# Kernel tuning notes

Measured on AMD Instinct MI355X. Metric: run time of the kernel, lower is better.

Reference implementation:

```python
import jax, jax.numpy as jnp
import numpy as np

N_LAYERS = 2
N_HIGHWAY = 2
WIDTH = 4
D = 256
B, S = 32, 1024


def setup_inputs() -> dict:
    key = jax.random.key(0)
    ks = jax.random.split(key, 10)
    inputs = jax.random.normal(ks[0], (B, S, D), dtype=jnp.float32)
    fwd_pad = jax.random.normal(ks[1], (N_LAYERS, WIDTH, D), dtype=jnp.float32) / np.sqrt(D)
    bwd_pad = jax.random.normal(ks[2], (N_LAYERS, WIDTH, D), dtype=jnp.float32) / np.sqrt(D)
    fwd_w = jax.random.normal(ks[3], (N_LAYERS, WIDTH + 1), dtype=jnp.float32)
    bwd_w = jax.random.normal(ks[4], (N_LAYERS, WIDTH + 1), dtype=jnp.float32)
    # Highway: each layer is Linear(D, 2D); chunk -> (nonlinear_part, gate)
    sc = 1.0 / np.sqrt(D)
    fwd_hw_W = jax.random.uniform(ks[5], (N_LAYERS, N_HIGHWAY, 2 * D, D), jnp.float32, -sc, sc)
    fwd_hw_b = jax.random.uniform(ks[6], (N_LAYERS, N_HIGHWAY, 2 * D), jnp.float32, -sc, sc)
    bwd_hw_W = jax.random.uniform(ks[7], (N_LAYERS, N_HIGHWAY, 2 * D, D), jnp.float32, -sc, sc)
    bwd_hw_b = jax.random.uniform(ks[8], (N_LAYERS, N_HIGHWAY, 2 * D), jnp.float32, -sc, sc)
    return {"inputs": inputs, "fwd_pad": fwd_pad, "bwd_pad": bwd_pad,
            "fwd_w": fwd_w, "bwd_w": bwd_w,
            "fwd_hw_W": fwd_hw_W, "fwd_hw_b": fwd_hw_b,
            "bwd_hw_W": bwd_hw_W, "bwd_hw_b": bwd_hw_b}


def _highway(x, Ws, bs):
    # AllenNLP-style Highway: gate*x + (1-gate)*relu(nonlinear_part)
    for l in range(Ws.shape[0]):
        proj = jnp.einsum('bsd,ed->bse', x, Ws[l]) + bs[l]
        nonlin, gate = jnp.split(proj, 2, axis=-1)
        g = jax.nn.sigmoid(gate)
        x = g * x + (1.0 - g) * jax.nn.relu(nonlin)
    return x


def reference(inputs, fwd_pad, bwd_pad, fwd_w, bwd_w, fwd_hw_W, fwd_hw_b, bwd_hw_W, bwd_hw_b):
    Bb, Ss, Dd = inputs.shape
    n_layers, width, _ = fwd_pad.shape
    fwd_x = inputs
    bwd_x = inputs
    outs = []
    for i in range(n_layers):
        front = jnp.broadcast_to(fwd_pad[i], (Bb, width, Dd))
        back = jnp.broadcast_to(bwd_pad[i], (Bb, width, Dd))
        pf = jnp.concatenate([front, fwd_x, back], axis=1)  # [B, S+2w, D]
        pb = jnp.concatenate([front, bwd_x, back], axis=1)
        # forward dir: window [start, start+width] of padded -> causal taps
        f = sum(fwd_w[i, j] * pf[:, j:j + Ss] for j in range(width + 1))
        # backward dir: window [start+width, start+2*width] -> anticausal taps
        b = sum(bwd_w[i, j] * pb[:, width + j:width + j + Ss] for j in range(width + 1))
        f = _highway(f, fwd_hw_W[i], fwd_hw_b[i])
        b = _highway(b, bwd_hw_W[i], bwd_hw_b[i])
        fwd_x, bwd_x = f, b
        outs.append(jnp.concatenate([f, b], axis=-1))
    return jnp.stack(outs, axis=0)  # [n_layers, B, S, 2D]
```

## Files before the change

kernel.cpp:

```cpp
#include <hip/hip_runtime.h>
#include <hip/hip_bf16.h>

#define S_LEN 1024
#define DM 256
#define NTOK 32768
#define OWN 56
#define NBLK 586
#define W_SLICE 16384
#define W_SUB   131072
#define W_LAYER 262144

typedef __attribute__((ext_vector_type(8))) short short8;
typedef __attribute__((ext_vector_type(4))) short s16x4;
typedef __attribute__((ext_vector_type(4))) float f32x4;

__device__ __forceinline__ float bf2f(unsigned short u) {
    return __uint_as_float(((unsigned int)u) << 16);
}
__device__ __forceinline__ short f2bf(float f) {
    __hip_bfloat16 h = __float2bfloat16(f);
    return *reinterpret_cast<short*>(&h);
}
__device__ __forceinline__ float sigmoid_fast(float x) {
    float e = __builtin_amdgcn_exp2f(x * -1.442695041f);
    return __builtin_amdgcn_rcpf(1.0f + e);
}

__global__ void convert_w_kernel(const float* __restrict__ WF,
                                 const float* __restrict__ WB,
                                 short* __restrict__ WbF,
                                 short* __restrict__ WbB) {
    int dirv = blockIdx.y;
    const float* src = dirv ? WB : WF;
    short* dst = dirv ? WbB : WbF;
    int idx = blockIdx.x * blockDim.x + threadIdx.x;
    int chunk = idx >> 14;
    int within = idx & 16383;
    int ks = within >> 11;
    int slot = within & 2047;
    int wvf = slot >> 6;
    int l = slot & 63;
    int wv = wvf >> 2;
    int f = wvf & 3;
    int lc = l & 15;
    int krow = l >> 4;
    int e = ((f >> 1) << 8) + wv * 32 + ((f & 1) << 4) + lc;
    int k0 = ks * 32 + krow * 8;
    const float* p = src + (size_t)chunk * W_SUB + (size_t)e * DM + k0;
    float4 a = *(const float4*)p;
    float4 b = *(const float4*)(p + 4);
    short8 v;
    v[0] = f2bf(a.x); v[1] = f2bf(a.y); v[2] = f2bf(a.z); v[3] = f2bf(a.w);
    v[4] = f2bf(b.x); v[5] = f2bf(b.y); v[6] = f2bf(b.z); v[7] = f2bf(b.w);
    *(short8*)(dst + (size_t)chunk * W_SUB + (size_t)ks * W_SLICE + (size_t)slot * 8) = v;
}

__device__ __forceinline__ void hw_sub(short* Xs, const short* __restrict__ Wsub,
                                       const float* __restrict__ bsub,
                                       int wv, int l, int lc, int krow) {
    f32x4 zero = {0.f, 0.f, 0.f, 0.f};
    f32x4 acc[4][4];
#pragma unroll
    for (int i = 0; i < 4; i++)
#pragma unroll
        for (int j = 0; j < 4; j++) acc[i][j] = zero;

    const short* wp = Wsub + (size_t)wv * 2048 + (size_t)l * 8;
    __builtin_amdgcn_s_setprio(1);
#pragma unroll 2
    for (int ks = 0; ks < 8; ks++) {
        const short* wk = wp + (size_t)ks * W_SLICE;
        short8 w0 = *(const short8*)(wk);
        short8 w1 = *(const short8*)(wk + 512);
        short8 w2 = *(const short8*)(wk + 1024);
        short8 w3 = *(const short8*)(wk + 1536);
        int k8 = ks * 4 + krow;
#pragma unroll
        for (int mf = 0; mf < 4; mf++) {
            int row = mf * 16 + lc;
            short8 a = *(const short8*)(Xs + row * DM + ((k8 ^ (row & 7)) << 3));
            acc[mf][0] = __builtin_amdgcn_mfma_f32_16x16x32_bf16(w0, a, acc[mf][0], 0, 0, 0);
            acc[mf][1] = __builtin_amdgcn_mfma_f32_16x16x32_bf16(w1, a, acc[mf][1], 0, 0, 0);
            acc[mf][2] = __builtin_amdgcn_mfma_f32_16x16x32_bf16(w2, a, acc[mf][2], 0, 0, 0);
            acc[mf][3] = __builtin_amdgcn_mfma_f32_16x16x32_bf16(w3, a, acc[mf][3], 0, 0, 0);
        }
    }
    __builtin_amdgcn_s_setprio(0);
    __syncthreads();

    const float* bsub2 = bsub + 256;
#pragma unroll
    for (int np = 0; np < 2; np++) {
        int e0 = wv * 32 + np * 16 + krow * 4;
        f32x4 bn = *(const f32x4*)(bsub + e0);
        f32x4 bg = *(const f32x4*)(bsub2 + e0);
#pragma unroll
        for (int mf = 0; mf < 4; mf++) {
            int t = mf * 16 + lc;
            int sx = t * DM + (((e0 >> 3) ^ (t & 7)) << 3) + (e0 & 7);
            s16x4 xv = *(const s16x4*)(Xs + sx);
            s16x4 yv;
#pragma unroll
            for (int r = 0; r < 4; r++) {
                float xe = bf2f((unsigned short)xv[r]);
                float nlv = acc[mf][np][r] + bn[r];
                float gv = acc[mf][np + 2][r] + bg[r];
                float g = sigmoid_fast(gv);
                float rl = fmaxf(nlv, 0.0f);
                float y = __builtin_fmaf(g, xe - rl, rl);
                yv[r] = f2bf(y);
            }
            *(s16x4*)(Xs + sx) = yv;
        }
    }
    __syncthreads();
}

__global__ __launch_bounds__(512, 4)
void bilm_kernel(const float* __restrict__ xin,
                 const float* __restrict__ fpad, const float* __restrict__ bpad,
                 const float* __restrict__ fw5, const float* __restrict__ bw5,
                 const short* __restrict__ WbF, const short* __restrict__ WbB,
                 const float* __restrict__ bF_, const float* __restrict__ bB_,
                 float* __restrict__ outp) {
    int dir = blockIdx.y;
    const short* Wd = dir ? WbB : WbF;
    const float* biasd = dir ? bB_ : bF_;
    const float* padd = dir ? bpad : fpad;
    const float* w5d = dir ? bw5 : fw5;
    int ch0 = dir ? 256 : 0;

    __shared__ __align__(16) short As[64 * DM];
    __shared__ __align__(16) short Bs[64 * DM];

    int tid = threadIdx.x;
    int wv = tid >> 6;
    int l = tid & 63;
    int lc = l & 15;
    int krow = l >> 4;
    int t0 = blockIdx.x * OWN;
    int base = t0 - 4;

    {
        float wj5[5];
#pragma unroll
        for (int j = 0; j < 5; j++) wj5[j] = w5d[j];
#pragma unroll
        for (int p = 0; p < 4; p++) {
            int pos = p * 512 + tid;
            int row = pos >> 5;
            int c = pos & 31;
            int d0 = c << 3;
            int tg = base + row;
            int s = tg & (S_LEN - 1);
            float a8[8];
#pragma unroll
            for (int i = 0; i < 8; i++) a8[i] = 0.0f;
#pragma unroll
            for (int j = 0; j < 5; j++) {
                float wj = wj5[j];
                bool use_pad = (dir == 0) ? (s + j < 4) : (s + j >= S_LEN);
                if (use_pad) {
                    const float* pf = (dir == 0) ? (padd + (size_t)(s + j) * DM + d0)
                                                 : (padd + (size_t)(s + j - S_LEN) * DM + d0);
                    const float4* q = (const float4*)pf;
                    float4 a = q[0], b = q[1];
                    a8[0] += wj * a.x; a8[1] += wj * a.y; a8[2] += wj * a.z; a8[3] += wj * a.w;
                    a8[4] += wj * b.x; a8[5] += wj * b.y; a8[6] += wj * b.z; a8[7] += wj * b.w;
                } else {
                    long st = (dir == 0) ? ((long)tg + j - 4) : ((long)tg + j);
                    st = st < 0 ? 0 : (st >= NTOK ? NTOK - 1 : st);
                    const float4* q = (const float4*)(xin + st * DM + d0);
                    float4 a = q[0], b = q[1];
                    a8[0] += wj * a.x; a8[1] += wj * a.y; a8[2] += wj * a.z; a8[3] += wj * a.w;
                    a8[4] += wj * b.x; a8[5] += wj * b.y; a8[6] += wj * b.z; a8[7] += wj * b.w;
                }
            }
            short8 o;
#pragma unroll
            for (int i = 0; i < 8; i++) o[i] = f2bf(a8[i]);
            *(short8*)(As + row * DM + ((c ^ (row & 7)) << 3)) = o;
        }
    }
    __syncthreads();

    hw_sub(As, Wd, biasd, wv, l, lc, krow);
    hw_sub(As, Wd + W_SUB, biasd + 512, wv, l, lc, krow);

    {
        float wj5[5];
#pragma unroll
        for (int j = 0; j < 5; j++) wj5[j] = w5d[5 + j];
        const float* padl1 = padd + 4 * DM;
#pragma unroll
        for (int p = 0; p < 4; p++) {
            int pos = p * 512 + tid;
            int row = pos >> 5;
            int c = pos & 31;
            int d0 = c << 3;
            int tg = base + row;
            int s = tg & (S_LEN - 1);
            float a8[8];
#pragma unroll
            for (int i = 0; i < 8; i++) a8[i] = 0.0f;
#pragma unroll
            for (int j = 0; j < 5; j++) {
                float wj = wj5[j];
                bool use_pad = (dir == 0) ? (s + j < 4) : (s + j >= S_LEN);
                if (use_pad) {
                    const float* pf = (dir == 0) ? (padl1 + (size_t)(s + j) * DM + d0)
                                                 : (padl1 + (size_t)(s + j - S_LEN) * DM + d0);
                    const float4* q = (const float4*)pf;
                    float4 a = q[0], b = q[1];
                    a8[0] += wj * a.x; a8[1] += wj * a.y; a8[2] += wj * a.z; a8[3] += wj * a.w;
                    a8[4] += wj * b.x; a8[5] += wj * b.y; a8[6] += wj * b.z; a8[7] += wj * b.w;
                } else {
                    int srow = (dir == 0) ? (row + j - 4) : (row + j);
                    srow = srow < 0 ? 0 : (srow > 63 ? 63 : srow);
                    short8 v = *(const short8*)(As + srow * DM + ((c ^ (srow & 7)) << 3));
#pragma unroll
                    for (int i = 0; i < 8; i++) a8[i] += wj * bf2f((unsigned short)v[i]);
                }
            }
            short8 o;
#pragma unroll
            for (int i = 0; i < 8; i++) o[i] = f2bf(a8[i]);
            *(short8*)(Bs + row * DM + ((c ^ (row & 7)) << 3)) = o;
        }
    }
    __syncthreads();

    hw_sub(Bs, Wd + W_LAYER, biasd + 1024, wv, l, lc, krow);
    hw_sub(Bs, Wd + W_LAYER + W_SUB, biasd + 1536, wv, l, lc, krow);

#pragma unroll
    for (int it = 0; it < 7; it++) {
        int pos = it * 512 + tid;
        int row = pos >> 6;
        int c4 = (pos & 63) << 2;
        int t = t0 + row;
        if (t < NTOK) {
            int lr = row + 4;
            int sx = lr * DM + (((c4 >> 3) ^ (lr & 7)) << 3) + (c4 & 7);
            s16x4 v0 = *(const s16x4*)(As + sx);
            s16x4 v1 = *(const s16x4*)(Bs + sx);
            float4 o0, o1;
            o0.x = bf2f((unsigned short)v0[0]); o0.y = bf2f((unsigned short)v0[1]);
            o0.z = bf2f((unsigned short)v0[2]); o0.w = bf2f((unsigned short)v0[3]);
            o1.x = bf2f((unsigned short)v1[0]); o1.y = bf2f((unsigned short)v1[1]);
            o1.z = bf2f((unsigned short)v1[2]); o1.w = bf2f((unsigned short)v1[3]);
            *(float4*)(outp + (size_t)t * 512 + ch0 + c4) = o0;
            *(float4*)(outp + (size_t)NTOK * 512 + (size_t)t * 512 + ch0 + c4) = o1;
        }
    }
}

extern "C" void kernel_launch(void* const* d_in, const int* in_sizes, int n_in,
                              void* d_out, int out_size, void* d_ws, size_t ws_size,
                              hipStream_t stream) {
    const float* inputs = (const float*)d_in[0];
    const float* fwd_pad = (const float*)d_in[1];
    const float* bwd_pad = (const float*)d_in[2];
    const float* fwd_w = (const float*)d_in[3];
    const float* bwd_w = (const float*)d_in[4];
    const float* fwd_hw_W = (const float*)d_in[5];
    const float* fwd_hw_b = (const float*)d_in[6];
    const float* bwd_hw_W = (const float*)d_in[7];
    const float* bwd_hw_b = (const float*)d_in[8];
    float* out = (float*)d_out;

    short* WbF = (short*)d_ws;
    short* WbB = WbF + (size_t)2 * W_LAYER;

    convert_w_kernel<<<dim3(256, 2), dim3(256), 0, stream>>>(fwd_hw_W, bwd_hw_W, WbF, WbB);

    bilm_kernel<<<dim3(NBLK, 2), dim3(512), 0, stream>>>(
        inputs, fwd_pad, bwd_pad, fwd_w, bwd_w,
        WbF, WbB, fwd_hw_b, bwd_hw_b, out);
}
```

Baseline: 121.1 us.

## Use one-sided halo per direction, fold sigmoid scale into weights, store layer-0 early

Each block of 64 rows keeps only a one-sided 4-row halo: causal for the forward direction and anticausal for the backward one. This lets each block own 60 tokens instead of 56, so fewer blocks are needed and less halo work is redone. The -log2(e) factor for the gate sigmoid is folded into the bf16 weight conversion and the bias, which removes a multiply from the epilogue. The layer-0 output is written to global memory right after its highway stage, so the store overlaps later compute and As is no longer read at the end. The weight scaling shifts bf16 rounding slightly, and the halo arithmetic must match the conv taps in each direction.

After: 127.2 us. 5.0% more time.

```diff
diff --git a/kernel.cpp b/kernel.cpp
--- a/kernel.cpp
+++ b/kernel.cpp
@@ -4,8 +4,8 @@
 #define S_LEN 1024
 #define DM 256
 #define NTOK 32768
-#define OWN 56
-#define NBLK 586
+#define OWN 60
+#define NBLK 547
 #define W_SLICE 16384
 #define W_SUB   131072
 #define W_LAYER 262144
@@ -14,16 +14,14 @@
 typedef __attribute__((ext_vector_type(4))) short s16x4;
 typedef __attribute__((ext_vector_type(4))) float f32x4;
 
+#define NLOG2E -1.442695041f
+
 __device__ __forceinline__ float bf2f(unsigned short u) {
     return __uint_as_float(((unsigned int)u) << 16);
 }
 __device__ __forceinline__ short f2bf(float f) {
     __hip_bfloat16 h = __float2bfloat16(f);
     return *reinterpret_cast<short*>(&h);
-}
-__device__ __forceinline__ float sigmoid_fast(float x) {
-    float e = __builtin_amdgcn_exp2f(x * -1.442695041f);
-    return __builtin_amdgcn_rcpf(1.0f + e);
 }
 
 __global__ void convert_w_kernel(const float* __restrict__ WF,
@@ -46,12 +44,13 @@
     int krow = l >> 4;
     int e = ((f >> 1) << 8) + wv * 32 + ((f & 1) << 4) + lc;
     int k0 = ks * 32 + krow * 8;
+    float sc = (f >> 1) ? NLOG2E : 1.0f;
     const float* p = src + (size_t)chunk * W_SUB + (size_t)e * DM + k0;
     float4 a = *(const float4*)p;
     float4 b = *(const float4*)(p + 4);
     short8 v;
-    v[0] = f2bf(a.x); v[1] = f2bf(a.y); v[2] = f2bf(a.z); v[3] = f2bf(a.w);
-    v[4] = f2bf(b.x); v[5] = f2bf(b.y); v[6] = f2bf(b.z); v[7] = f2bf(b.w);
+    v[0] = f2bf(sc * a.x); v[1] = f2bf(sc * a.y); v[2] = f2bf(sc * a.z); v[3] = f2bf(sc * a.w);
+    v[4] = f2bf(sc * b.x); v[5] = f2bf(sc * b.y); v[6] = f2bf(sc * b.z); v[7] = f2bf(sc * b.w);
     *(short8*)(dst + (size_t)chunk * W_SUB + (size_t)ks * W_SLICE + (size_t)slot * 8) = v;
 }
 
@@ -93,7 +92,10 @@
     for (int np = 0; np < 2; np++) {
         int e0 = wv * 32 + np * 16 + krow * 4;
         f32x4 bn = *(const f32x4*)(bsub + e0);
-        f32x4 bg = *(const f32x4*)(bsub2 + e0);
+        f32x4 bgr = *(const f32x4*)(bsub2 + e0);
+        f32x4 bg;
+#pragma unroll
+        for (int r = 0; r < 4; r++) bg[r] = NLOG2E * bgr[r];
 #pragma unroll
         for (int mf = 0; mf < 4; mf++) {
             int t = mf * 16 + lc;
@@ -105,7 +107,7 @@
                 float xe = bf2f((unsigned short)xv[r]);
                 float nlv = acc[mf][np][r] + bn[r];
                 float gv = acc[mf][np + 2][r] + bg[r];
-                float g = sigmoid_fast(gv);
+                float g = __builtin_amdgcn_rcpf(1.0f + __builtin_amdgcn_exp2f(gv));
                 float rl = fmaxf(nlv, 0.0f);
                 float y = __builtin_fmaf(g, xe - rl, rl);
                 yv[r] = f2bf(y);
@@ -139,7 +141,8 @@
     int lc = l & 15;
     int krow = l >> 4;
     int t0 = blockIdx.x * OWN;
-    int base = t0 - 4;
+    int hoff = (dir == 0) ? 4 : 0;
+    int base = t0 - hoff;
 
     {
         float wj5[5];
@@ -187,6 +190,25 @@
     hw_sub(As, Wd, biasd, wv, l, lc, krow);
     hw_sub(As, Wd + W_SUB, biasd + 512, wv, l, lc, krow);
 
+#pragma unroll
+    for (int it = 0; it < 8; it++) {
+        int pos = it * 512 + tid;
+        if (pos < OWN * 64) {
+            int row = pos >> 6;
+            int c4 = (pos & 63) << 2;
+            int t = t0 + row;
+            if (t < NTOK) {
+                int lr = row + hoff;
+                int sx = lr * DM + (((c4 >> 3) ^ (lr & 7)) << 3) + (c4 & 7);
+                s16x4 v0 = *(const s16x4*)(As + sx);
+                float4 o0;
+                o0.x = bf2f((unsigned short)v0[0]); o0.y = bf2f((unsigned short)v0[1]);
+                o0.z = bf2f((unsigned short)v0[2]); o0.w = bf2f((unsigned short)v0[3]);
+                *(float4*)(outp + (size_t)t * 512 + ch0 + c4) = o0;
+            }
+        }
+    }
+
     {
         float wj5[5];
 #pragma unroll
@@ -234,23 +256,21 @@
     hw_sub(Bs, Wd + W_LAYER + W_SUB, biasd + 1536, wv, l, lc, krow);
 
 #pragma unroll
-    for (int it = 0; it < 7; it++) {
+    for (int it = 0; it < 8; it++) {
         int pos = it * 512 + tid;
-        int row = pos >> 6;
-        int c4 = (pos & 63) << 2;
-        int t = t0 + row;
-        if (t < NTOK) {
-            int lr = row + 4;
-            int sx = lr * DM + (((c4 >> 3) ^ (lr & 7)) << 3) + (c4 & 7);
-            s16x4 v0 = *(const s16x4*)(As + sx);
-            s16x4 v1 = *(const s16x4*)(Bs + sx);
-            float4 o0, o1;
-            o0.x = bf2f((unsigned short)v0[0]); o0.y = bf2f((unsigned short)v0[1]);
-            o0.z = bf2f((unsigned short)v0[2]); o0.w = bf2f((unsigned short)v0[3]);
-            o1.x = bf2f((unsigned short)v1[0]); o1.y = bf2f((unsigned short)v1[1]);
-            o1.z = bf2f((unsigned short)v1[2]); o1.w = bf2f((unsigned short)v1[3]);
-            *(float4*)(outp + (size_t)t * 512 + ch0 + c4) = o0;
-            *(float4*)(outp + (size_t)NTOK * 512 + (size_t)t * 512 + ch0 + c4) = o1;
+        if (pos < OWN * 64) {
+            int row = pos >> 6;
+            int c4 = (pos & 63) << 2;
+            int t = t0 + row;
+            if (t < NTOK) {
+                int lr = row + hoff;
+                int sx = lr * DM + (((c4 >> 3) ^ (lr & 7)) << 3) + (c4 & 7);
+                s16x4 v1 = *(const s16x4*)(Bs + sx);
+                float4 o1;
+                o1.x = bf2f((unsigned short)v1[0]); o1.y = bf2f((unsigned short)v1[1]);
+                o1.z = bf2f((unsigned short)v1[2]); o1.w = bf2f((unsigned short)v1[3]);
+                *(float4*)(outp + (size_t)NTOK * 512 + (size_t)t * 512 + ch0 + c4) = o1;
+            }
         }
     }
 }
```
